# Kernel optimization log

Measured on AMD Instinct MI355X. Metric: run time of the kernel, lower is better.

The kernel has to match this reference:

```python
import jax, jax.numpy as jnp
import numpy as np

D_CONV = 4
D_STATE = 16
DT_RANK = 64  # ceil(1024/16)


def _forward(x, W_in, conv_w, conv_b, W_x, W_dt, b_dt, A_log, Dp, W_out):
    B, L, Dm = x.shape
    d_inner = W_dt.shape[0]
    # in_proj: (B,L,Dm) @ (2*d_inner, Dm)^T
    xz = jnp.einsum('bld,ed->ble', x, W_in)
    xc, z = jnp.split(xz, 2, axis=-1)  # each (B,L,d_inner)
    # depthwise causal conv1d (torch pads both sides by d_conv-1 then truncates to L == left-pad only)
    xt = jnp.swapaxes(xc, 1, 2)  # (B, d_inner, L)
    conv = jax.lax.conv_general_dilated(
        xt, conv_w[:, None, :], window_strides=(1,),
        padding=[(D_CONV - 1, 0)], feature_group_count=d_inner)
    xconv = jax.nn.silu(jnp.swapaxes(conv, 1, 2) + conv_b)  # (B,L,d_inner)
    # x_proj -> dt_low, B, C
    x_dbl = jnp.einsum('bld,ed->ble', xconv, W_x)
    dt_low = x_dbl[..., :DT_RANK]
    Bp = x_dbl[..., DT_RANK:DT_RANK + D_STATE]      # (B,L,N)
    Cp = x_dbl[..., DT_RANK + D_STATE:]             # (B,L,N)
    dt = jax.nn.softplus(jnp.einsum('blr,dr->bld', dt_low, W_dt) + b_dt)  # (B,L,d_inner)
    A = -jnp.exp(A_log)  # (d_inner, N)

    # recurrence h_t = exp(dt_t * A) * h_{t-1} + dt_t * B_t * x_t ; y_t = <h_t, C_t>
    def step(h, inp):
        dt_t, B_t, C_t, x_t = inp  # (B,D),(B,N),(B,N),(B,D)
        dA = jnp.exp(dt_t[..., None] * A)                      # (B,D,N)
        dBx = dt_t[..., None] * B_t[:, None, :] * x_t[..., None]
        h = dA * h + dBx
        y = jnp.einsum('bdn,bn->bd', h, C_t)
        return h, y

    h0 = jnp.zeros((B, d_inner, D_STATE), dtype=x.dtype)
    xs = (jnp.swapaxes(dt, 0, 1), jnp.swapaxes(Bp, 0, 1),
          jnp.swapaxes(Cp, 0, 1), jnp.swapaxes(xconv, 0, 1))
    _, ys = jax.lax.scan(step, h0, xs)  # ys: (L,B,d_inner)
    y = jnp.swapaxes(ys, 0, 1) + xconv * Dp  # skip connection with D
    out = jnp.einsum('bld,ed->ble', y * jax.nn.silu(z), W_out)
    return out


def setup_inputs() -> dict:
    key = jax.random.key(0)
    ks = jax.random.split(key, 8)
    B, L, d_model = 2, 1024, 1024
    d_inner = 2 * d_model
    x = jax.random.normal(ks[0], (B, L, d_model), dtype=jnp.float32)
    W_in = jax.random.normal(ks[1], (2 * d_inner, d_model), dtype=jnp.float32) / np.sqrt(d_model)
    conv_w = jax.random.normal(ks[2], (d_inner, D_CONV), dtype=jnp.float32) / np.sqrt(D_CONV)
    conv_b = jnp.zeros((d_inner,), dtype=jnp.float32)
    W_x = jax.random.normal(ks[3], (DT_RANK + 2 * D_STATE, d_inner), dtype=jnp.float32) / np.sqrt(d_inner)
    W_dt = jax.random.uniform(ks[4], (d_inner, DT_RANK), minval=-1.0, maxval=1.0, dtype=jnp.float32) * DT_RANK ** -0.5
    dt = jnp.exp(jax.random.uniform(ks[5], (d_inner,), dtype=jnp.float32)
                 * (np.log(0.1) - np.log(0.001)) + np.log(0.001))
    b_dt = dt + jnp.log(-jnp.expm1(-dt))  # softplus inverse init
    A_log = jnp.log(jnp.tile(jnp.arange(1, D_STATE + 1, dtype=jnp.float32), (d_inner, 1)))
    Dp = jnp.ones((d_inner,), dtype=jnp.float32)
    W_out = jax.random.normal(ks[6], (d_model, d_inner), dtype=jnp.float32) / np.sqrt(d_inner)
    return {'x': x, 'W_in': W_in, 'conv_w': conv_w, 'conv_b': conv_b, 'W_x': W_x,
            'W_dt': W_dt, 'b_dt': b_dt, 'A_log': A_log, 'Dp': Dp, 'W_out': W_out}


def reference(x, W_in, conv_w, conv_b, W_x, W_dt, b_dt, A_log, Dp, W_out):
    return _forward(x, W_in, conv_w, conv_b, W_x, W_dt, b_dt, A_log, Dp, W_out)
```

## Files before the change

### kernel.cpp

```cpp
#include <hip/hip_runtime.h>
#include <hip/hip_bf16.h>
#include <math.h>

constexpr int Bb  = 2;
constexpr int Ls  = 1024;
constexpr int DM  = 1024;
constexpr int DI  = 2048;
constexpr int DXZ = 4096;
constexpr int DXD = 96;
constexpr int DTR = 64;
constexpr int DST = 16;
constexpr int NCH = 8;
constexpr int CHL = 128;
constexpr int ML  = Bb * Ls;

typedef __attribute__((ext_vector_type(8))) short bf16x8;
typedef __attribute__((ext_vector_type(4))) float f32x4;

__device__ __forceinline__ float sigmoidf_(float v) {
    return 1.0f / (1.0f + __expf(-v));
}

__device__ __forceinline__ int pk_bf16(float lo, float hi) {
    unsigned int ul = __float_as_uint(lo);
    ul += 0x7fffu + ((ul >> 16) & 1u);
    unsigned int uh = __float_as_uint(hi);
    uh += 0x7fffu + ((uh >> 16) & 1u);
    return (int)((ul >> 16) | (uh & 0xffff0000u));
}

template <int CTRL>
__device__ __forceinline__ float dpp_add_(float v) {
    int t = __builtin_amdgcn_update_dpp(
        0, __float_as_int(v), CTRL, 0xF, 0xF, true);
    return v + __int_as_float(t);
}
__device__ __forceinline__ float red16_(float p) {
    p = dpp_add_<0xB1>(p);
    p = dpp_add_<0x4E>(p);
    p = dpp_add_<0x141>(p);
    p = dpp_add_<0x140>(p);
    return p;
}

__device__ __forceinline__ int swz(int row, int chunk) {
    return (((row << 2) + chunk) ^ (row & 7)) << 3;
}

template <int SPLIT, int ABF16>
__global__ __launch_bounds__(256) void gemm_bf16_f32in(
    const void* __restrict__ Av, int lda,
    const float* __restrict__ W, int ldw,
    float* __restrict__ C, float* __restrict__ C2, int ldc, int K,
    int za, int zw, long zc)
{
    __shared__ __align__(16) unsigned short As[128 * 32];
    __shared__ __align__(16) unsigned short Ws[128 * 32];

    const int tid  = threadIdx.x;
    const int lane = tid & 63;
    const int wave = tid >> 6;
    const int bm = blockIdx.y * 128;
    const int bn = blockIdx.x * 128;
    const int z  = blockIdx.z;
    C += (size_t)z * zc;

    const int srow = tid >> 1;
    const int cb   = (tid & 1) * 2;
    const float* Ag = (ABF16 ? nullptr
        : (const float*)Av + (size_t)z * za + (size_t)(bm + srow) * lda + cb * 8);
    const unsigned short* Ag16 = (ABF16
        ? (const unsigned short*)Av + (size_t)z * za
          + (size_t)(bm + srow) * lda + cb * 8 : nullptr);
    const float* Wg = W + (size_t)z * zw + (size_t)(bn + srow) * ldw + cb * 8;
    const int ia0 = swz(srow, cb);
    const int ia1 = swz(srow, cb + 1);

    const int wr = (wave >> 1) * 64;
    const int wc = (wave & 1) * 64;
    const int fr = lane & 15;
    const int fq = lane >> 4;

    f32x4 acc[4][4];
#pragma unroll
    for (int m = 0; m < 4; ++m)
#pragma unroll
        for (int n = 0; n < 4; ++n) acc[m][n] = (f32x4){0.f, 0.f, 0.f, 0.f};

    for (int k0 = 0; k0 < K; k0 += 32) {
        int4 pa0, pa1;
        if (ABF16) {
            pa0 = *(const int4*)(Ag16 + k0);
            pa1 = *(const int4*)(Ag16 + k0 + 8);
        } else {
            const float4 a0 = *(const float4*)(Ag + k0);
            const float4 a1 = *(const float4*)(Ag + k0 + 4);
            const float4 a2 = *(const float4*)(Ag + k0 + 8);
            const float4 a3 = *(const float4*)(Ag + k0 + 12);
            pa0 = (int4){pk_bf16(a0.x, a0.y), pk_bf16(a0.z, a0.w),
                         pk_bf16(a1.x, a1.y), pk_bf16(a1.z, a1.w)};
            pa1 = (int4){pk_bf16(a2.x, a2.y), pk_bf16(a2.z, a2.w),
                         pk_bf16(a3.x, a3.y), pk_bf16(a3.z, a3.w)};
        }
        const float4 w0 = *(const float4*)(Wg + k0);
        const float4 w1 = *(const float4*)(Wg + k0 + 4);
        const float4 w2 = *(const float4*)(Wg + k0 + 8);
        const float4 w3 = *(const float4*)(Wg + k0 + 12);

        __syncthreads();
        {
            const int4 pw0 = {pk_bf16(w0.x, w0.y), pk_bf16(w0.z, w0.w),
                              pk_bf16(w1.x, w1.y), pk_bf16(w1.z, w1.w)};
            const int4 pw1 = {pk_bf16(w2.x, w2.y), pk_bf16(w2.z, w2.w),
                              pk_bf16(w3.x, w3.y), pk_bf16(w3.z, w3.w)};
            *(int4*)(As + ia0) = pa0;
            *(int4*)(As + ia1) = pa1;
            *(int4*)(Ws + ia0) = pw0;
            *(int4*)(Ws + ia1) = pw1;
        }
        __syncthreads();

        bf16x8 af[4], bfv[4];
#pragma unroll
        for (int m = 0; m < 4; ++m)
            af[m] = *(const bf16x8*)(As + swz(wr + m * 16 + fr, fq));
#pragma unroll
        for (int n = 0; n < 4; ++n)
            bfv[n] = *(const bf16x8*)(Ws + swz(wc + n * 16 + fr, fq));
#pragma unroll
        for (int m = 0; m < 4; ++m)
#pragma unroll
            for (int n = 0; n < 4; ++n)
                acc[m][n] = __builtin_amdgcn_mfma_f32_16x16x32_bf16(
                    af[m], bfv[n], acc[m][n], 0, 0, 0);
    }

#pragma unroll
    for (int m = 0; m < 4; ++m)
#pragma unroll
        for (int n = 0; n < 4; ++n) {
            const int col = bn + wc + n * 16 + fr;
#pragma unroll
            for (int j = 0; j < 4; ++j) {
                const int row = bm + wr + m * 16 + fq * 4 + j;
                const float v = acc[m][n][j];
                if (SPLIT) {
                    if (col < DI) {
                        C[(size_t)row * ldc + col] = v;
                    } else {
                        C2[(size_t)row * ldc + (col - DI)] = v * sigmoidf_(v);
                    }
                } else {
                    C[(size_t)row * ldc + col] = v;
                }
            }
        }
}

__global__ __launch_bounds__(256) void reduce4_kernel(
    const float* __restrict__ part, float* __restrict__ out, int n4)
{
    const int i = blockIdx.x * 256 + threadIdx.x;
    if (i >= n4) return;
    const size_t stride = (size_t)ML * DM;
    float4 a = *(const float4*)(part + (size_t)i * 4);
    const float4 b = *(const float4*)(part + stride + (size_t)i * 4);
    const float4 c = *(const float4*)(part + 2 * stride + (size_t)i * 4);
    const float4 d = *(const float4*)(part + 3 * stride + (size_t)i * 4);
    a.x += b.x + c.x + d.x;
    a.y += b.y + c.y + d.y;
    a.z += b.z + c.z + d.z;
    a.w += b.w + c.w + d.w;
    *(float4*)(out + (size_t)i * 4) = a;
}

template <int EPI, int ATRANS>
__global__ __launch_bounds__(256) void gemm_nt(
    const float* __restrict__ A, int lda,
    const float* __restrict__ W, int ldw,
    float* __restrict__ C, int ldc,
    int N, int K, const float* __restrict__ bias, int za, int zw, int zc)
{
    A += (size_t)blockIdx.z * za;
    W += (size_t)blockIdx.z * zw;
    C += (size_t)blockIdx.z * zc;

    __shared__ float Asl[16][132];
    __shared__ float Wsl[16][132];

    const int tid = threadIdx.x;
    const int tx = tid & 15;
    const int ty = tid >> 4;
    const int bm = blockIdx.y * 128;
    const int bn = blockIdx.x * 128;

    const int lr = tid >> 1;
    const int lk = (tid & 1) * 8;
    const int krow = tid >> 4;
    const int mseg = (tid & 15) * 8;

    float acc[8][8];
#pragma unroll
    for (int i = 0; i < 8; ++i)
#pragma unroll
        for (int j = 0; j < 8; ++j) acc[i][j] = 0.0f;

    const float* Ap = ATRANS
        ? A + (size_t)krow * lda + bm + mseg
        : A + (size_t)(bm + lr) * lda + lk;
    const float* Wp = W + (size_t)(bn + lr) * ldw + lk;
    const bool wok = (bn + lr) < N;
    const float4 f4z = make_float4(0.f, 0.f, 0.f, 0.f);

    for (int k0 = 0; k0 < K; k0 += 16) {
        float4 av0, av1;
        if (ATRANS) {
            av0 = *(const float4*)(Ap + (size_t)k0 * lda);
            av1 = *(const float4*)(Ap + (size_t)k0 * lda + 4);
        } else {
            av0 = *(const float4*)(Ap + k0);
            av1 = *(const float4*)(Ap + k0 + 4);
        }
        const float4 wv0 = wok ? *(const float4*)(Wp + k0)     : f4z;
        const float4 wv1 = wok ? *(const float4*)(Wp + k0 + 4) : f4z;

        __syncthreads();
        if (ATRANS) {
            *(float4*)&Asl[krow][mseg]     = av0;
            *(float4*)&Asl[krow][mseg + 4] = av1;
        } else {
            Asl[lk + 0][lr] = av0.x; Asl[lk + 1][lr] = av0.y;
            Asl[lk + 2][lr] = av0.z; Asl[lk + 3][lr] = av0.w;
            Asl[lk + 4][lr] = av1.x; Asl[lk + 5][lr] = av1.y;
            Asl[lk + 6][lr] = av1.z; Asl[lk + 7][lr] = av1.w;
        }
        Wsl[lk + 0][lr] = wv0.x; Wsl[lk + 1][lr] = wv0.y;
        Wsl[lk + 2][lr] = wv0.z; Wsl[lk + 3][lr] = wv0.w;
        Wsl[lk + 4][lr] = wv1.x; Wsl[lk + 5][lr] = wv1.y;
        Wsl[lk + 6][lr] = wv1.z; Wsl[lk + 7][lr] = wv1.w;
        __syncthreads();

#pragma unroll
        for (int k = 0; k < 16; ++k) {
            const float4 a0 = *(const float4*)&Asl[k][(ty << 2)];
            const float4 a1 = *(const float4*)&Asl[k][64 + (ty << 2)];
            const float4 b0 = *(const float4*)&Wsl[k][(tx << 2)];
            const float4 b1 = *(const float4*)&Wsl[k][64 + (tx << 2)];
            const float ar[8] = {a0.x, a0.y, a0.z, a0.w, a1.x, a1.y, a1.z, a1.w};
            const float br[8] = {b0.x, b0.y, b0.z, b0.w, b1.x, b1.y, b1.z, b1.w};
#pragma unroll
            for (int i = 0; i < 8; ++i)
#pragma unroll
                for (int j = 0; j < 8; ++j)
                    acc[i][j] = fmaf(ar[i], br[j], acc[i][j]);
        }
    }

#pragma unroll
    for (int i = 0; i < 8; ++i) {
        const int row = bm + ((i & 4) << 4) + (ty << 2) + (i & 3);
#pragma unroll
        for (int j = 0; j < 8; ++j) {
            const int col = bn + ((j & 4) << 4) + (tx << 2) + (j & 3);
            if (col < N) {
                float v = acc[i][j];
                if (EPI == 2) {
                    v += bias[row];
                    v = (v > 20.f) ? v : log1pf(__expf(v));
                }
                C[(size_t)row * ldc + col] = v;
            }
        }
    }
}

__global__ __launch_bounds__(256) void reduce_xdbl_kernel(
    const float* __restrict__ part, float* __restrict__ xdbl,
    float* __restrict__ bcT)
{
    const int idx = blockIdx.x * 256 + threadIdx.x;
    if (idx >= ML * DXD) return;
    const int m = idx / DXD;
    const int j = idx - m * DXD;
    const float* p = part + (size_t)m * 768 + j;
    float s = 0.0f;
#pragma unroll
    for (int kc = 0; kc < 8; ++kc) s += p[kc * DXD];
    xdbl[idx] = s;
    if (j >= DTR) bcT[(size_t)(j - DTR) * ML + m] = s;
}

constexpr int CT_LDS = 260;
__global__ __launch_bounds__(256) void conv_transpose_kernel(
    const float* __restrict__ xc,
    const float* __restrict__ conv_w,
    const float* __restrict__ conv_b,
    float* __restrict__ xT)
{
    __shared__ float tile[32][CT_LDS];
    const int d0 = blockIdx.x * 32;
    const int m0 = blockIdx.y * 256;
    const int t  = threadIdx.x;
    const bool atStart = ((m0 & (Ls - 1)) == 0);

    for (int rg = 0; rg < 33; ++rg) {
        const int r = rg * 8 + (t >> 5) - 3;
        const int dcol = t & 31;
        if (r <= 255) {
            float v = 0.0f;
            if (r >= 0 || !atStart)
                v = xc[(size_t)(m0 + r) * DI + d0 + dcol];
            tile[dcol][3 + r] = v;
        }
    }
    __syncthreads();

    const int dd  = t >> 3;
    const int seg = (t & 7) * 32;
    const int d   = d0 + dd;
    const float4 cw = *(const float4*)(conv_w + (d << 2));
    const float  cb = conv_b[d];
    float* dst = xT + (size_t)d * ML + m0 + seg;

    float4 cur = *(const float4*)&tile[dd][seg];
#pragma unroll
    for (int g = 0; g < 8; ++g) {
        const float4 nxt = *(const float4*)&tile[dd][seg + 4 * g + 4];
        const float a0 = cb + cw.x*cur.x + cw.y*cur.y + cw.z*cur.z + cw.w*cur.w;
        const float a1 = cb + cw.x*cur.y + cw.y*cur.z + cw.z*cur.w + cw.w*nxt.x;
        const float a2 = cb + cw.x*cur.z + cw.y*cur.w + cw.z*nxt.x + cw.w*nxt.y;
        const float a3 = cb + cw.x*cur.w + cw.y*nxt.x + cw.z*nxt.y + cw.w*nxt.z;
        float4 o;
        o.x = a0 * sigmoidf_(a0); o.y = a1 * sigmoidf_(a1);
        o.z = a2 * sigmoidf_(a2); o.w = a3 * sigmoidf_(a3);
        *(float4*)(dst + 4 * g) = o;
        cur = nxt;
    }
}

__global__ __launch_bounds__(256) void scan_pass1(
    const float* __restrict__ dtT,
    const float* __restrict__ xT,
    const float* __restrict__ bcT,
    const float* __restrict__ A_log,
    float* __restrict__ hend, float* __restrict__ Dprod)
{
    const int b    = blockIdx.z;
    const int c    = blockIdx.y;
    const int lane = threadIdx.x & 63;
    const int wave = threadIdx.x >> 6;
    const int n    = lane & 15;
    const int dl   = lane >> 4;
    const int d    = blockIdx.x * 16 + wave * 4 + dl;
    const int m0   = b * Ls + c * CHL;

    const float Anat = -__expf(A_log[(d << 4) + n]);

    const float4* dtp = (const float4*)(dtT + (size_t)d * ML + m0);
    const float4* xp  = (const float4*)(xT  + (size_t)d * ML + m0);
    const float4* Bp  = (const float4*)(bcT + (size_t)n * ML + m0);

    float4 dt4 = dtp[0], x4 = xp[0], B4 = Bp[0];
    float h = 0.0f, S = 0.0f;

    for (int it = 0; it < CHL / 4; ++it) {
        const float4 dtc = dt4, xc4 = x4, Bc = B4;
        if (it + 1 < CHL / 4) {
            dt4 = dtp[it + 1]; x4 = xp[it + 1]; B4 = Bp[it + 1];
        }
#pragma unroll
        for (int i = 0; i < 4; ++i) {
            const float dtv = ((const float*)&dtc)[i];
            const float xv  = ((const float*)&xc4)[i];
            const float Bn  = ((const float*)&Bc)[i];
            S += dtv;
            const float e = __expf(dtv * Anat);
            h = fmaf(e, h, dtv * xv * Bn);
        }
    }

    const size_t idx = (((size_t)(b * NCH + c) * DI + d) << 4) + n;
    hend[idx]  = h;
    Dprod[idx] = __expf(Anat * S);
}

__global__ __launch_bounds__(256) void scan_pass2(
    const float* __restrict__ dtT,
    float* xT,
    const float* __restrict__ bcT,
    const float* __restrict__ A_log,
    const float* __restrict__ Dp,
    const float* __restrict__ hend, const float* __restrict__ Dprod)
{
    const int b    = blockIdx.z;
    const int c    = blockIdx.y;
    const int lane = threadIdx.x & 63;
    const int wave = threadIdx.x >> 6;
    const int n    = lane & 15;
    const int dl   = lane >> 4;
    const int d    = blockIdx.x * 16 + wave * 4 + dl;
    const int m0   = b * Ls + c * CHL;

    const float Anat = -__expf(A_log[(d << 4) + n]);
    const float dpd  = Dp[d];

    float h = 0.0f;
    for (int cp = 0; cp < c; ++cp) {
        const size_t off = (((size_t)(b * NCH + cp) * DI + d) << 4) + n;
        h = fmaf(Dprod[off], h, hend[off]);
    }

    const float4* dtp = (const float4*)(dtT + (size_t)d * ML + m0);
    const float4* xp  = (const float4*)(xT  + (size_t)d * ML + m0);
    const float4* Bp  = (const float4*)(bcT + (size_t)n * ML + m0);
    const float4* Cp  = (const float4*)(bcT + (size_t)(DST + n) * ML + m0);
    float4* yq = (float4*)(xT + (size_t)d * ML + m0);

    float4 dt4 = dtp[0], x4 = xp[0], B4 = Bp[0], C4 = Cp[0];

    for (int it = 0; it < CHL / 4; ++it) {
        const float4 dtc = dt4, xc4 = x4, Bc = B4, Cc = C4;
        if (it + 1 < CHL / 4) {
            dt4 = dtp[it + 1]; x4 = xp[it + 1];
            B4 = Bp[it + 1];   C4 = Cp[it + 1];
        }
        float4 y4;
#pragma unroll
        for (int i = 0; i < 4; ++i) {
            const float dtv = ((const float*)&dtc)[i];
            const float xv  = ((const float*)&xc4)[i];
            const float Bn  = ((const float*)&Bc)[i];
            const float Cn  = ((const float*)&Cc)[i];
            const float e = __expf(dtv * Anat);
            h = fmaf(e, h, dtv * xv * Bn);
            const float p = red16_(h * Cn);
            ((float*)&y4)[i] = fmaf(xv, dpd, p);
        }
        if (n == 0) yq[it] = y4;
    }
}

__global__ __launch_bounds__(256) void gate_transpose_kernel(
    const float* __restrict__ yT,
    const float* __restrict__ zg,
    unsigned short* __restrict__ yb)
{
    __shared__ float Ty[64][65];
    __shared__ float Tz[64][65];
    const int d0 = blockIdx.x * 64;
    const int m0 = blockIdx.y * 64;
    const int t  = threadIdx.x;
    const int cc = t & 63, r4 = t >> 6;

#pragma unroll 4
    for (int rr = 0; rr < 16; ++rr) {
        const int r = rr * 4 + r4;
        Ty[r][cc] = yT[(size_t)(d0 + r) * ML + m0 + cc];
        Tz[r][cc] = zg[(size_t)(m0 + r) * DI + d0 + cc];
    }
    __syncthreads();

    const int dp  = (t & 31) * 2;
    const int mr4 = t >> 5;
#pragma unroll 4
    for (int rr = 0; rr < 8; ++rr) {
        const int mr = rr * 8 + mr4;
        const float v0 = Ty[dp][mr]     * Tz[mr][dp];
        const float v1 = Ty[dp + 1][mr] * Tz[mr][dp + 1];
        *(unsigned int*)(yb + (size_t)(m0 + mr) * DI + d0 + dp) =
            (unsigned int)pk_bf16(v0, v1);
    }
}

extern "C" void kernel_launch(void* const* d_in, const int* in_sizes, int n_in,
                              void* d_out, int out_size, void* d_ws, size_t ws_size,
                              hipStream_t stream)
{
    const float* x      = (const float*)d_in[0];
    const float* W_in   = (const float*)d_in[1];
    const float* conv_w = (const float*)d_in[2];
    const float* conv_b = (const float*)d_in[3];
    const float* W_x    = (const float*)d_in[4];
    const float* W_dt   = (const float*)d_in[5];
    const float* b_dt   = (const float*)d_in[6];
    const float* A_log  = (const float*)d_in[7];
    const float* Dp     = (const float*)d_in[8];
    const float* W_out  = (const float*)d_in[9];
    float* out = (float*)d_out;

    float* ws     = (float*)d_ws;
    float* xc_arr = ws;
    float* zg_arr = xc_arr + (size_t)ML * DI;
    float* xT_arr = zg_arr + (size_t)ML * DI;
    float* xdbl   = xT_arr + (size_t)ML * DI;

    float* hend  = out;
    float* Dprod = hend + (size_t)Bb * NCH * DI * DST;
    float* bcT   = Dprod + (size_t)Bb * NCH * DI * DST;

    float* dtT = xc_arr;
    unsigned short* ybf = (unsigned short*)xc_arr;
    float* oPart = zg_arr;

    const dim3 blk(256);

    gemm_bf16_f32in<1, 0><<<dim3(DXZ / 128, ML / 128), blk, 0, stream>>>(
        x, DM, W_in, DM, xc_arr, zg_arr, DI, DM, 0, 0, 0);

    conv_transpose_kernel<<<dim3(DI / 32, ML / 256), blk, 0, stream>>>(
        xc_arr, conv_w, conv_b, xT_arr);

    gemm_nt<0, 1><<<dim3(1, ML / 128, 8), blk, 0, stream>>>(
        xT_arr, ML, W_x, DI, xc_arr, 768, DXD, DI / 8, nullptr,
        (DI / 8) * ML, DI / 8, DXD);
    reduce_xdbl_kernel<<<dim3((ML * DXD + 255) / 256), blk, 0, stream>>>(
        xc_arr, xdbl, bcT);

    gemm_nt<2, 0><<<dim3(ML / 128, DI / 128), blk, 0, stream>>>(
        W_dt, DTR, xdbl, DXD, dtT, ML, ML, DTR, b_dt, 0, 0, 0);

    scan_pass1<<<dim3(DI / 16, NCH - 1, Bb), blk, 0, stream>>>(
        dtT, xT_arr, bcT, A_log, hend, Dprod);
    scan_pass2<<<dim3(DI / 16, NCH, Bb), blk, 0, stream>>>(
        dtT, xT_arr, bcT, A_log, Dp, hend, Dprod);

    gate_transpose_kernel<<<dim3(DI / 64, ML / 64), blk, 0, stream>>>(
        xT_arr, zg_arr, ybf);

    gemm_bf16_f32in<0, 1><<<dim3(DM / 128, ML / 128, 4), blk, 0, stream>>>(
        ybf, DI, W_out, DI, oPart, nullptr, DM, DI / 4,
        DI / 4, DI / 4, (long)ML * DM);

    reduce4_kernel<<<dim3((ML * DM / 4 + 255) / 256), blk, 0, stream>>>(
        oPart, out, ML * DM / 4);
}
```

Baseline: 411.3 us.

## Pre-convert GEMM operands to bf16 and double scan chunk count

Adds a standalone fp32-to-bf16 conversion kernel. x, W_in and W_out are converted once per call, so the in_proj and out_proj GEMMs load bf16 operands directly instead of converting fp32 tiles inside the main loop, where each W_in tile is re-read and re-converted by every block row. The scan chunking changes from 8×128 to 16×64 for more parallelism in the chunked scan. Workspace layout is reshuffled so that dt_low and B/C get dedicated buffers, since hend/Dprod now grow and take over the space in out. The cost is extra launches and extra memory traffic for the conversion passes.

```diff
diff --git a/kernel.cpp b/kernel.cpp
--- a/kernel.cpp
+++ b/kernel.cpp
@@ -10,8 +10,8 @@
 constexpr int DXD = 96;
 constexpr int DTR = 64;
 constexpr int DST = 16;
-constexpr int NCH = 8;
-constexpr int CHL = 128;
+constexpr int NCH = 16;
+constexpr int CHL = 64;
 constexpr int ML  = Bb * Ls;
 
 typedef __attribute__((ext_vector_type(8))) short bf16x8;
@@ -47,10 +47,20 @@
     return (((row << 2) + chunk) ^ (row & 7)) << 3;
 }
 
-template <int SPLIT, int ABF16>
+__global__ __launch_bounds__(256) void cvt_bf16_kernel(
+    const float* __restrict__ in, unsigned short* __restrict__ out, int n4)
+{
+    const int i = blockIdx.x * 256 + threadIdx.x;
+    if (i >= n4) return;
+    const float4 v = *(const float4*)(in + (size_t)i * 4);
+    *(int2*)(out + (size_t)i * 4) =
+        make_int2(pk_bf16(v.x, v.y), pk_bf16(v.z, v.w));
+}
+
+template <int SPLIT, int ABF16, int WBF16>
 __global__ __launch_bounds__(256) void gemm_bf16_f32in(
     const void* __restrict__ Av, int lda,
-    const float* __restrict__ W, int ldw,
+    const void* __restrict__ Wv, int ldw,
     float* __restrict__ C, float* __restrict__ C2, int ldc, int K,
     int za, int zw, long zc)
 {
@@ -72,7 +82,11 @@
     const unsigned short* Ag16 = (ABF16
         ? (const unsigned short*)Av + (size_t)z * za
           + (size_t)(bm + srow) * lda + cb * 8 : nullptr);
-    const float* Wg = W + (size_t)z * zw + (size_t)(bn + srow) * ldw + cb * 8;
+    const float* Wg = (WBF16 ? nullptr
+        : (const float*)Wv + (size_t)z * zw + (size_t)(bn + srow) * ldw + cb * 8);
+    const unsigned short* Wg16 = (WBF16
+        ? (const unsigned short*)Wv + (size_t)z * zw
+          + (size_t)(bn + srow) * ldw + cb * 8 : nullptr);
     const int ia0 = swz(srow, cb);
     const int ia1 = swz(srow, cb + 1);
 
@@ -88,7 +102,7 @@
         for (int n = 0; n < 4; ++n) acc[m][n] = (f32x4){0.f, 0.f, 0.f, 0.f};
 
     for (int k0 = 0; k0 < K; k0 += 32) {
-        int4 pa0, pa1;
+        int4 pa0, pa1, pw0, pw1;
         if (ABF16) {
             pa0 = *(const int4*)(Ag16 + k0);
             pa1 = *(const int4*)(Ag16 + k0 + 8);
@@ -102,22 +116,25 @@
             pa1 = (int4){pk_bf16(a2.x, a2.y), pk_bf16(a2.z, a2.w),
                          pk_bf16(a3.x, a3.y), pk_bf16(a3.z, a3.w)};
         }
-        const float4 w0 = *(const float4*)(Wg + k0);
-        const float4 w1 = *(const float4*)(Wg + k0 + 4);
-        const float4 w2 = *(const float4*)(Wg + k0 + 8);
-        const float4 w3 = *(const float4*)(Wg + k0 + 12);
+        if (WBF16) {
+            pw0 = *(const int4*)(Wg16 + k0);
+            pw1 = *(const int4*)(Wg16 + k0 + 8);
+        } else {
+            const float4 w0 = *(const float4*)(Wg + k0);
+            const float4 w1 = *(const float4*)(Wg + k0 + 4);
+            const float4 w2 = *(const float4*)(Wg + k0 + 8);
+            const float4 w3 = *(const float4*)(Wg + k0 + 12);
+            pw0 = (int4){pk_bf16(w0.x, w0.y), pk_bf16(w0.z, w0.w),
+                         pk_bf16(w1.x, w1.y), pk_bf16(w1.z, w1.w)};
+            pw1 = (int4){pk_bf16(w2.x, w2.y), pk_bf16(w2.z, w2.w),
+                         pk_bf16(w3.x, w3.y), pk_bf16(w3.z, w3.w)};
+        }
 
         __syncthreads();
-        {
-            const int4 pw0 = {pk_bf16(w0.x, w0.y), pk_bf16(w0.z, w0.w),
-                              pk_bf16(w1.x, w1.y), pk_bf16(w1.z, w1.w)};
-            const int4 pw1 = {pk_bf16(w2.x, w2.y), pk_bf16(w2.z, w2.w),
-                              pk_bf16(w3.x, w3.y), pk_bf16(w3.z, w3.w)};
-            *(int4*)(As + ia0) = pa0;
-            *(int4*)(As + ia1) = pa1;
-            *(int4*)(Ws + ia0) = pw0;
-            *(int4*)(Ws + ia1) = pw1;
-        }
+        *(int4*)(As + ia0) = pa0;
+        *(int4*)(As + ia1) = pa1;
+        *(int4*)(Ws + ia0) = pw0;
+        *(int4*)(Ws + ia1) = pw1;
         __syncthreads();
 
         bf16x8 af[4], bfv[4];
@@ -275,7 +292,7 @@
 }
 
 __global__ __launch_bounds__(256) void reduce_xdbl_kernel(
-    const float* __restrict__ part, float* __restrict__ xdbl,
+    const float* __restrict__ part, float* __restrict__ dtlow,
     float* __restrict__ bcT)
 {
     const int idx = blockIdx.x * 256 + threadIdx.x;
@@ -286,8 +303,8 @@
     float s = 0.0f;
 #pragma unroll
     for (int kc = 0; kc < 8; ++kc) s += p[kc * DXD];
-    xdbl[idx] = s;
-    if (j >= DTR) bcT[(size_t)(j - DTR) * ML + m] = s;
+    if (j < DTR) dtlow[(size_t)m * DTR + j] = s;
+    else         bcT[(size_t)(j - DTR) * ML + m] = s;
 }
 
 constexpr int CT_LDS = 260;
@@ -492,20 +509,28 @@
     float* xc_arr = ws;
     float* zg_arr = xc_arr + (size_t)ML * DI;
     float* xT_arr = zg_arr + (size_t)ML * DI;
-    float* xdbl   = xT_arr + (size_t)ML * DI;
+    float* dtlow  = xT_arr + (size_t)ML * DI;
+    float* bcT    = dtlow  + (size_t)ML * DTR;
 
     float* hend  = out;
     float* Dprod = hend + (size_t)Bb * NCH * DI * DST;
-    float* bcT   = Dprod + (size_t)Bb * NCH * DI * DST;
-
+
+    unsigned short* xbf  = (unsigned short*)xT_arr;
+    unsigned short* wibf = xbf + (size_t)ML * DM;
     float* dtT = xc_arr;
-    unsigned short* ybf = (unsigned short*)xc_arr;
+    unsigned short* ybf  = (unsigned short*)xc_arr;
+    unsigned short* wobf = (unsigned short*)xc_arr + (size_t)ML * DI;
     float* oPart = zg_arr;
 
     const dim3 blk(256);
 
-    gemm_bf16_f32in<1, 0><<<dim3(DXZ / 128, ML / 128), blk, 0, stream>>>(
-        x, DM, W_in, DM, xc_arr, zg_arr, DI, DM, 0, 0, 0);
+    cvt_bf16_kernel<<<dim3(ML * DM / 4 / 256), blk, 0, stream>>>(
+        x, xbf, ML * DM / 4);
+    cvt_bf16_kernel<<<dim3(DXZ * DM / 4 / 256), blk, 0, stream>>>(
+        W_in, wibf, DXZ * DM / 4);
+
+    gemm_bf16_f32in<1, 1, 1><<<dim3(DXZ / 128, ML / 128), blk, 0, stream>>>(
+        xbf, DM, wibf, DM, xc_arr, zg_arr, DI, DM, 0, 0, 0);
 
     conv_transpose_kernel<<<dim3(DI / 32, ML / 256), blk, 0, stream>>>(
         xc_arr, conv_w, conv_b, xT_arr);
@@ -514,10 +539,10 @@
         xT_arr, ML, W_x, DI, xc_arr, 768, DXD, DI / 8, nullptr,
         (DI / 8) * ML, DI / 8, DXD);
     reduce_xdbl_kernel<<<dim3((ML * DXD + 255) / 256), blk, 0, stream>>>(
-        xc_arr, xdbl, bcT);
+        xc_arr, dtlow, bcT);
 
     gemm_nt<2, 0><<<dim3(ML / 128, DI / 128), blk, 0, stream>>>(
-        W_dt, DTR, xdbl, DXD, dtT, ML, ML, DTR, b_dt, 0, 0, 0);
+        W_dt, DTR, dtlow, DTR, dtT, ML, ML, DTR, b_dt, 0, 0, 0);
 
     scan_pass1<<<dim3(DI / 16, NCH - 1, Bb), blk, 0, stream>>>(
         dtT, xT_arr, bcT, A_log, hend, Dprod);
@@ -526,9 +551,11 @@
 
     gate_transpose_kernel<<<dim3(DI / 64, ML / 64), blk, 0, stream>>>(
         xT_arr, zg_arr, ybf);
-
-    gemm_bf16_f32in<0, 1><<<dim3(DM / 128, ML / 128, 4), blk, 0, stream>>>(
-        ybf, DI, W_out, DI, oPart, nullptr, DM, DI / 4,
+    cvt_bf16_kernel<<<dim3(DM * DI / 4 / 256), blk, 0, stream>>>(
+        W_out, wobf, DM * DI / 4);
+
+    gemm_bf16_f32in<0, 1, 1><<<dim3(DM / 128, ML / 128, 4), blk, 0, stream>>>(
+        ybf, DI, wobf, DI, oPart, nullptr, DM, DI / 4,
         DI / 4, DI / 4, (long)ML * DM);
 
     reduce4_kernel<<<dim3((ML * DM / 4 + 255) / 256), blk, 0, stream>>>(
```

After: 409.2 us. Within noise of the previous version (-0.5%).
